# Optimization experiments

Hardware: AMD Instinct MI355X
Metric: run time of the kernel (lower is better)

The kernel has to match this reference:

```python
import jax, jax.numpy as jnp
import numpy as np
import math

NUM_HEADS = 16
HEAD_DIM = 128
ROPE_BASE = 10000.0


def setup_inputs() -> dict:
    key = jax.random.key(0)
    ks = jax.random.split(key, 6)
    B, S, H = 2, 2048, 2048
    hidden_states = jax.random.normal(ks[0], (B, S, H), dtype=jnp.float32) * 0.02
    # causal additive mask, shape (B, 1, S, S)
    neg = jnp.finfo(jnp.float32).min
    causal = jnp.where(jnp.tril(jnp.ones((S, S), dtype=bool)), 0.0, neg).astype(jnp.float32)
    attention_mask = jnp.broadcast_to(causal[None, None], (B, 1, S, S))
    position_ids = jnp.broadcast_to(jnp.arange(S, dtype=jnp.int64)[None], (B, S))
    scale = 1.0 / math.sqrt(H)
    Wq = jax.random.normal(ks[1], (H, H), dtype=jnp.float32) * scale
    Wk = jax.random.normal(ks[2], (H, H), dtype=jnp.float32) * scale
    Wv = jax.random.normal(ks[3], (H, H), dtype=jnp.float32) * scale
    Wo = jax.random.normal(ks[4], (H, H), dtype=jnp.float32) * scale
    return {"hidden_states": hidden_states, "attention_mask": attention_mask,
            "position_ids": position_ids, "Wq": Wq, "Wk": Wk, "Wv": Wv, "Wo": Wo}


def _rotate_half(x):
    x1, x2 = jnp.split(x, 2, axis=-1)
    return jnp.concatenate((-x2, x1), axis=-1)


def reference(hidden_states, attention_mask, position_ids, Wq, Wk, Wv, Wo):
    B, S, H = hidden_states.shape
    nh, hd = NUM_HEADS, HEAD_DIM

    def shape_heads(x):  # (B,S,H) -> (B,nh,S,hd)
        return x.reshape(B, S, nh, hd).transpose(0, 2, 1, 3)

    q = shape_heads(hidden_states @ Wq.T)
    k = shape_heads(hidden_states @ Wk.T)
    v = shape_heads(hidden_states @ Wv.T)

    kv_seq_len = S  # no past_key_value
    # rotary table: (kv_seq_len, hd)
    inv_freq = 1.0 / (ROPE_BASE ** (jnp.arange(0, hd, 2, dtype=jnp.float32) / hd))
    t = jnp.arange(kv_seq_len, dtype=jnp.float32)
    freqs = jnp.einsum('i,j->ij', t, inv_freq)
    emb = jnp.concatenate((freqs, freqs), axis=-1)
    # gather-based RoPE == table lookup at position_ids: (B,S,hd) -> (B,1,S,hd)
    cos = jnp.cos(emb)[position_ids][:, None]
    sin = jnp.sin(emb)[position_ids][:, None]

    q = q * cos + _rotate_half(q) * sin
    k = k * cos + _rotate_half(k) * sin

    scores = jnp.einsum('bhqd,bhkd->bhqk', q, k) / math.sqrt(hd)
    scores = scores + attention_mask
    scores = jnp.maximum(scores, jnp.finfo(scores.dtype).min)
    probs = jax.nn.softmax(scores.astype(jnp.float32), axis=-1).astype(q.dtype)
    attn = jnp.einsum('bhqk,bhkd->bhqd', probs, v)  # (B,nh,S,hd)
    attn = attn.transpose(0, 2, 1, 3).reshape(B, S, H)
    return attn @ Wo.T
```

## Files before the change

kernel.cpp:

```cpp
#include <hip/hip_runtime.h>
#include <hip/hip_bf16.h>
#include <cstdint>

#define SQ    2048
#define HDIM  2048
#define NH    16
#define HD    128
#define BATCH 2
#define MTOK  (BATCH*SQ)

typedef unsigned short u16;
typedef unsigned int   u32;
typedef __bf16 bf16x8 __attribute__((ext_vector_type(8)));
typedef float  f32x4  __attribute__((ext_vector_type(4)));
typedef float  f32x16 __attribute__((ext_vector_type(16)));
typedef unsigned short u16x4 __attribute__((ext_vector_type(4)));
typedef unsigned int   u32x4 __attribute__((ext_vector_type(4)));

__device__ __forceinline__ u16 f2b(float f) {
  union { float f; unsigned u; } v; v.f = f;
  return (u16)((v.u + 0x7fffu + ((v.u >> 16) & 1u)) >> 16);
}
__device__ __forceinline__ float b2f(u16 b) {
  union { unsigned u; float f; } v; v.u = ((unsigned)b) << 16;
  return v.f;
}

#define GLD_LDS16(gp, lp) __builtin_amdgcn_global_load_lds( \
    (const __attribute__((address_space(1))) uint32_t*)(gp), \
    (__attribute__((address_space(3))) uint32_t*)(lp), 16, 0, 0)

__device__ __forceinline__ f32x16 zero16() {
  f32x16 v;
#pragma unroll
  for (int i = 0; i < 16; ++i) v[i] = 0.f;
  return v;
}

__global__ __launch_bounds__(256) void conv_bf16(const float* __restrict__ in,
                                                 u16* __restrict__ out, int n4) {
  int i = blockIdx.x * 256 + threadIdx.x;
  if (i >= n4) return;
  float4 v = ((const float4*)in)[i];
  u16x4 o;
  o.x = f2b(v.x); o.y = f2b(v.y); o.z = f2b(v.z); o.w = f2b(v.w);
  *(u16x4*)(out + (size_t)i * 4) = o;
}

__global__ __launch_bounds__(256) void conv_w4(const float* __restrict__ w0,
                                               const float* __restrict__ w1,
                                               const float* __restrict__ w2,
                                               const float* __restrict__ w3,
                                               u16* o0, u16* o1, u16* o2, u16* o3) {
  int i = blockIdx.x * 256 + threadIdx.x;
  int sel = blockIdx.y;
  const float* in = sel == 0 ? w0 : sel == 1 ? w1 : sel == 2 ? w2 : w3;
  u16* out = sel == 0 ? o0 : sel == 1 ? o1 : sel == 2 ? o2 : o3;
  float4 v = ((const float4*)in)[i];
  u16x4 o;
  o.x = f2b(v.x); o.y = f2b(v.y); o.z = f2b(v.z); o.w = f2b(v.w);
  *(u16x4*)(out + (size_t)i * 4) = o;
}

__global__ __launch_bounds__(256) void addk(const float* __restrict__ a,
                                            const float* __restrict__ b,
                                            float* __restrict__ o) {
  int i = blockIdx.x * 256 + threadIdx.x;
  float4 x = ((const float4*)a)[i], y = ((const float4*)b)[i];
  float4 r; r.x = x.x + y.x; r.y = x.y + y.y; r.z = x.z + y.z; r.w = x.w + y.w;
  ((float4*)o)[i] = r;
}

__global__ void rope_table_k(float* __restrict__ ct, float* __restrict__ st) {
  int s = blockIdx.x, j = threadIdx.x;
  float invf = expf(-(float)j * (9.210340371976184f / 64.0f));
  float ang = (float)s * invf;
  ct[s * 64 + j] = cosf(ang);
  st[s * 64 + j] = sinf(ang);
}

__global__ __launch_bounds__(256) void rope_apply2(u16* __restrict__ Xq,
                                                   u16* __restrict__ Xk,
                                                   const float* __restrict__ ct,
                                                   const float* __restrict__ st) {
  u16* X = blockIdx.y ? Xk : Xq;
  int idx = blockIdx.x * 256 + threadIdx.x;
  int j = idx & 63;
  int row = idx >> 6;
  int s = row & (SQ - 1);
  size_t base = (size_t)row * HD;
  float x1 = b2f(X[base + j]), x2 = b2f(X[base + j + 64]);
  float c = ct[s * 64 + j], sn = st[s * 64 + j];
  X[base + j]      = f2b(x1 * c - x2 * sn);
  X[base + j + 64] = f2b(x2 * c + x1 * sn);
}

template<int OUT>
__global__ __launch_bounds__(512, 1)
void gemm8m(const u16* __restrict__ A, const u16* __restrict__ W0,
            const u16* __restrict__ W1, const u16* __restrict__ W2,
            u16* __restrict__ oQ, u16* __restrict__ oK, u16* __restrict__ oV,
            float* __restrict__ oF, float* __restrict__ oF2, int nt) {
  __shared__ u16 Ah[2][2][128 * 64];
  __shared__ u16 Bh[2][2][128 * 64];
  const int tid = threadIdx.x, lane = tid & 63, w = tid >> 6;
  const int wm = w >> 2, wn = w & 3;
  const int gx = gridDim.x;
  const int lin = blockIdx.y * gx + blockIdx.x;
  const int cpx = (gx * gridDim.y) >> 3;
  const int swz = (lin & 7) * cpx + (lin >> 3);
  const int bx = swz % gx, by = swz / gx;
  const int m0 = by * 256;
  const int n0g = bx * 256;
  const int kbase = (OUT == 1) ? (int)blockIdx.z * 1024 : 0;
  int sel; const u16* Bw; int nloc;
  if (OUT == 0) {
    sel = n0g >> 11;
    Bw = (sel == 0) ? W0 : (sel == 1) ? W1 : W2;
    nloc = n0g & 2047;
  } else {
    sel = 0; Bw = W0; nloc = n0g;
  }
  float* dstF = (OUT == 1) ? (blockIdx.z ? oF2 : oF) : oF;

  u32 aoff[2][2], boff[2][2];
#pragma unroll
  for (int h = 0; h < 2; ++h) {
#pragma unroll
    for (int l = 0; l < 2; ++l) {
      int c = l * 512 + tid, ra = c >> 3, sl = c & 7;
      int r = ((ra >> 6) << 7) + h * 64 + (ra & 63);
      aoff[h][l] = (u32)((m0 + r) * HDIM + kbase + ((sl ^ (ra & 7)) * 8));
      int col = nloc + ((ra >> 5) * 64) + h * 32 + (ra & 31);
      boff[h][l] = (u32)(col * HDIM + kbase + ((sl ^ (ra & 7)) * 8));
    }
  }
  auto stageA = [&](int buf, int h, int k0) {
#pragma unroll
    for (int l = 0; l < 2; ++l)
      GLD_LDS16(A + (size_t)aoff[h][l] + k0, &Ah[buf][h][(l * 512 + tid) * 8]);
  };
  auto stageB = [&](int buf, int h, int k0) {
#pragma unroll
    for (int l = 0; l < 2; ++l)
      GLD_LDS16(Bw + (size_t)boff[h][l] + k0, &Bh[buf][h][(l * 512 + tid) * 8]);
  };

  f32x4 acc[8][4];
#pragma unroll
  for (int i = 0; i < 8; ++i)
#pragma unroll
    for (int j = 0; j < 4; ++j) acc[i][j] = (f32x4){0.f, 0.f, 0.f, 0.f};

  const int l15 = lane & 15, hi4 = lane >> 4;
  const int swr = (l15 & 7) << 4;

  bf16x8 afv0[4][2], afv1[4][2];
  bf16x8 bfv0[2][2], bfv1[2][2];

  auto readA = [&](bf16x8 (&dst)[4][2], const char* Ab) {
#pragma unroll
    for (int j = 0; j < 4; ++j)
#pragma unroll
      for (int kk = 0; kk < 2; ++kk)
        dst[j][kk] = *(const bf16x8*)(Ab + (wm * 64 + j * 16 + l15) * 128 +
                                      ((kk * 64 + hi4 * 16) ^ swr));
  };
  auto readB = [&](bf16x8 (&dst)[2][2], const char* Bb) {
#pragma unroll
    for (int j2 = 0; j2 < 2; ++j2)
#pragma unroll
      for (int kk = 0; kk < 2; ++kk)
        dst[j2][kk] = *(const bf16x8*)(Bb + (wn * 32 + j2 * 16 + l15) * 128 +
                                       ((kk * 64 + hi4 * 16) ^ swr));
  };
  auto mfq = [&](bf16x8 (&af)[4][2], bf16x8 (&bf)[2][2], int mh, int nh) {
#pragma unroll
    for (int kk = 0; kk < 2; ++kk)
#pragma unroll
      for (int j = 0; j < 4; ++j)
#pragma unroll
        for (int j2 = 0; j2 < 2; ++j2)
          acc[mh * 4 + j][nh * 2 + j2] = __builtin_amdgcn_mfma_f32_16x16x32_bf16(
              af[j][kk], bf[j2][kk], acc[mh * 4 + j][nh * 2 + j2], 0, 0, 0);
  };

  stageA(0, 0, 0); stageB(0, 0, 0); stageA(0, 1, 0); stageB(0, 1, 0);
  asm volatile("s_waitcnt vmcnt(4)" ::: "memory");
  __builtin_amdgcn_s_barrier();

  for (int t = 0; t < nt; ++t) {
    const int cur = t & 1, nb = cur ^ 1;
    const bool st = (t + 1 < nt);
    const int kn = (t + 1) * 64;
    const char* Ab0 = (const char*)&Ah[cur][0][0];
    const char* Ab1 = (const char*)&Ah[cur][1][0];
    const char* Bb0 = (const char*)&Bh[cur][0][0];
    const char* Bb1 = (const char*)&Bh[cur][1][0];

    readA(afv0, Ab0); readB(bfv0, Bb0);
    if (st) {
      stageA(nb, 0, kn); stageB(nb, 0, kn);
      asm volatile("s_waitcnt vmcnt(6)" ::: "memory");
    } else {
      asm volatile("s_waitcnt vmcnt(2)" ::: "memory");
    }
    __builtin_amdgcn_s_barrier();
    asm volatile("s_waitcnt lgkmcnt(0)" ::: "memory");
    __builtin_amdgcn_sched_barrier(0);
    __builtin_amdgcn_s_setprio(1); mfq(afv0, bfv0, 0, 0); __builtin_amdgcn_s_setprio(0);

    readA(afv1, Ab1);
    if (st) {
      stageA(nb, 1, kn);
      asm volatile("s_waitcnt vmcnt(6)" ::: "memory");
    } else {
      asm volatile("s_waitcnt vmcnt(0)" ::: "memory");
    }
    __builtin_amdgcn_s_barrier();
    asm volatile("s_waitcnt lgkmcnt(0)" ::: "memory");
    __builtin_amdgcn_sched_barrier(0);
    __builtin_amdgcn_s_setprio(1); mfq(afv1, bfv0, 1, 0); __builtin_amdgcn_s_setprio(0);

    readB(bfv1, Bb1);
    if (st) stageB(nb, 1, kn);
    __builtin_amdgcn_s_barrier();
    asm volatile("s_waitcnt lgkmcnt(0)" ::: "memory");
    __builtin_amdgcn_sched_barrier(0);
    __builtin_amdgcn_s_setprio(1); mfq(afv0, bfv1, 0, 1); __builtin_amdgcn_s_setprio(0);

    if (st) asm volatile("s_waitcnt vmcnt(4)" ::: "memory");
    __builtin_amdgcn_s_barrier();
    __builtin_amdgcn_s_setprio(1); mfq(afv1, bfv1, 1, 1); __builtin_amdgcn_s_setprio(0);
  }

  const int cl = l15, rg = hi4 * 4;
#pragma unroll
  for (int mi = 0; mi < 8; ++mi) {
#pragma unroll
    for (int ni = 0; ni < 4; ++ni) {
      const int mb = m0 + wm * 128 + mi * 16 + rg;
      const int n = nloc + wn * 64 + ni * 16 + cl;
      if (OUT == 1) {
#pragma unroll
        for (int r = 0; r < 4; ++r)
          dstF[(size_t)(mb + r) * HDIM + n] = acc[mi][ni][r];
      } else {
        const int h = n >> 7, d = n & 127;
        if (sel == 2) {
          const int b = mb >> 11, s = mb & (SQ - 1);
          u16x4 pk;
          pk.x = f2b(acc[mi][ni][0]); pk.y = f2b(acc[mi][ni][1]);
          pk.z = f2b(acc[mi][ni][2]); pk.w = f2b(acc[mi][ni][3]);
          *(u16x4*)&oV[((size_t)(b * NH + h) * HD + d) * SQ + s] = pk;
        } else {
          u16* O = sel ? oK : oQ;
#pragma unroll
          for (int r = 0; r < 4; ++r) {
            const int m = mb + r, b = m >> 11, s = m & (SQ - 1);
            O[((size_t)(b * NH + h) * SQ + s) * HD + d] = f2b(acc[mi][ni][r]);
          }
        }
      }
    }
  }
}

__device__ __forceinline__ void stage_kv(u16* ksb, u16* vsb,
                                         const u16* __restrict__ Kg,
                                         const u16* __restrict__ Vg,
                                         int kv0, int w, int lane) {
#pragma unroll
  for (int i = 0; i < 4; ++i) {
    int chunk = (w * 4 + i) * 64 + lane;
    int row = chunk >> 4, c16 = chunk & 15;
    int csrc = c16 ^ (row & 7);
    GLD_LDS16(Kg + (size_t)(kv0 + row) * HD + csrc * 8, ksb + (w * 4 + i) * 512);
  }
#pragma unroll
  for (int i = 0; i < 4; ++i) {
    int chunk = (w * 4 + i) * 64 + lane;
    int d = chunk >> 3, c8 = chunk & 7;
    int csrc = c8 ^ (d & 7);
    GLD_LDS16(Vg + (size_t)d * SQ + kv0 + csrc * 8, vsb + (w * 4 + i) * 512);
  }
}

#define MKPA(dst, P, off) { \
  u32 u0_, u1_, u2_, u3_; \
  asm("v_cvt_pk_bf16_f32 %0, %1, %2" : "=v"(u0_) : "v"(P[off + 0]), "v"(P[off + 1])); \
  asm("v_cvt_pk_bf16_f32 %0, %1, %2" : "=v"(u1_) : "v"(P[off + 2]), "v"(P[off + 3])); \
  asm("v_cvt_pk_bf16_f32 %0, %1, %2" : "=v"(u2_) : "v"(P[off + 4]), "v"(P[off + 5])); \
  asm("v_cvt_pk_bf16_f32 %0, %1, %2" : "=v"(u3_) : "v"(P[off + 6]), "v"(P[off + 7])); \
  u32 x0_ = (u32)__shfl_xor((int)u0_, 32, 64); \
  u32 x1_ = (u32)__shfl_xor((int)u1_, 32, 64); \
  u32 x2_ = (u32)__shfl_xor((int)u2_, 32, 64); \
  u32 x3_ = (u32)__shfl_xor((int)u3_, 32, 64); \
  u32x4 w_; \
  w_.x = hi ? x2_ : u0_; \
  w_.y = hi ? x3_ : u1_; \
  w_.z = hi ? u2_ : x0_; \
  w_.w = hi ? u3_ : x1_; \
  dst = __builtin_bit_cast(bf16x8, w_); \
}

#define PVD(oD, dblk) { \
  const int dr_ = (dblk) * 32 + l31; \
  const int sw_ = (dr_ & 7) << 4; \
  bf16x8 v0_ = *(const bf16x8*)(Vb + ((dr_ * 128 +  0 + hi * 16) ^ sw_)); \
  oD = __builtin_amdgcn_mfma_f32_32x32x16_bf16(pa[0], v0_, oD, 0, 0, 0); \
  bf16x8 v1_ = *(const bf16x8*)(Vb + ((dr_ * 128 + 32 + hi * 16) ^ sw_)); \
  oD = __builtin_amdgcn_mfma_f32_32x32x16_bf16(pa[1], v1_, oD, 0, 0, 0); \
  bf16x8 v2_ = *(const bf16x8*)(Vb + ((dr_ * 128 + 64 + hi * 16) ^ sw_)); \
  oD = __builtin_amdgcn_mfma_f32_32x32x16_bf16(pa[2], v2_, oD, 0, 0, 0); \
  bf16x8 v3_ = *(const bf16x8*)(Vb + ((dr_ * 128 + 96 + hi * 16) ^ sw_)); \
  oD = __builtin_amdgcn_mfma_f32_32x32x16_bf16(pa[3], v3_, oD, 0, 0, 0); \
}

__global__ __launch_bounds__(256, 2)
void flash_fwd2(const u16* __restrict__ Q, const u16* __restrict__ K,
                const u16* __restrict__ Vt, u16* __restrict__ Out) {
  __shared__ u16 Ks[2][64 * 128];
  __shared__ u16 Vs[2][128 * 64];
  const int tid = threadIdx.x, lane = tid & 63, w = tid >> 6;
  const int hi = lane >> 5, l31 = lane & 31;
  const int qt = 15 - (int)(blockIdx.x >> 5);
  const int bh = blockIdx.x & 31;
  const int q0 = qt * 128;
  const u16* Qg = Q + (size_t)bh * SQ * HD;
  const u16* Kg = K + (size_t)bh * SQ * HD;
  const u16* Vg = Vt + (size_t)bh * HD * SQ;
  const int qw = q0 + w * 32;
  const int qg = qw + l31;

  bf16x8 qf[8];
#pragma unroll
  for (int st = 0; st < 8; ++st)
    qf[st] = *(const bf16x8*)&Qg[(size_t)qg * HD + st * 16 + hi * 8];

  f32x16 o0 = zero16(), o1 = zero16(), o2 = zero16(), o3 = zero16();
  float lsum = 0.f;
  const float sL2E = 0.1275174446f;
  const int ktl = 2 * qt + 1;
  int cur = 0;

  stage_kv(Ks[0], Vs[0], Kg, Vg, 0, w, lane);

  for (int kt = 0; kt <= ktl; ++kt) {
    if (kt < ktl) {
      stage_kv(Ks[cur ^ 1], Vs[cur ^ 1], Kg, Vg, (kt + 1) * 64, w, lane);
      asm volatile("s_waitcnt vmcnt(8)" ::: "memory");
    } else {
      asm volatile("s_waitcnt vmcnt(0)" ::: "memory");
    }
    __builtin_amdgcn_s_barrier();

    const int kv0 = kt * 64;
    if (kv0 <= qw + 31) {
      const char* Kb = (const char*)Ks[cur];
      const char* Vb = (const char*)Vs[cur];
      f32x16 c0 = zero16(), c1 = zero16();
      const int kr0 = l31, kr1 = 32 + l31;
      const int sw0 = (kr0 & 7) << 4;
#pragma unroll
      for (int st = 0; st < 8; ++st) {
        bf16x8 k0 = *(const bf16x8*)(Kb + ((kr0 * 256 + st * 32 + hi * 16) ^ sw0));
        c0 = __builtin_amdgcn_mfma_f32_32x32x16_bf16(k0, qf[st], c0, 0, 0, 0);
        bf16x8 k1 = *(const bf16x8*)(Kb + ((kr1 * 256 + st * 32 + hi * 16) ^ sw0));
        c1 = __builtin_amdgcn_mfma_f32_32x32x16_bf16(k1, qf[st], c1, 0, 0, 0);
      }
      const bool needmask = (kv0 + 63 > qw);
      const int lim0 = qg - kv0, lim1 = lim0 - 32;
      if (needmask) {
#pragma unroll
        for (int r = 0; r < 16; ++r) {
          const int cr = (r & 3) + 8 * (r >> 2) + 4 * hi;
          float p0 = exp2f(c0[r] * sL2E);
          c0[r] = (cr <= lim0) ? p0 : 0.f;
          float p1 = exp2f(c1[r] * sL2E);
          c1[r] = (cr <= lim1) ? p1 : 0.f;
          lsum += c0[r] + c1[r];
        }
      } else {
#pragma unroll
        for (int r = 0; r < 16; ++r) {
          c0[r] = exp2f(c0[r] * sL2E);
          c1[r] = exp2f(c1[r] * sL2E);
          lsum += c0[r] + c1[r];
        }
      }
      bf16x8 pa[4];
      MKPA(pa[0], c0, 0); MKPA(pa[1], c0, 8);
      MKPA(pa[2], c1, 0); MKPA(pa[3], c1, 8);
      PVD(o0, 0) PVD(o1, 1) PVD(o2, 2) PVD(o3, 3)
    }
    __builtin_amdgcn_s_barrier();
    cur ^= 1;
  }

  float ltot = lsum + __shfl_xor(lsum, 32, 64);
  float invl = 1.f / ltot;
  const int b = bh >> 4, h = bh & 15;
#pragma unroll
  for (int g = 0; g < 4; ++g) {
#pragma unroll
    for (int j = 0; j < 4; ++j) {
      const int r = g * 4 + j;
      const int cr = g * 8 + 4 * hi + j;
      float inv = __shfl(invl, cr, 64);
      const int s = q0 + w * 32 + cr;
      size_t rb = ((size_t)(b * SQ + s)) * HDIM + h * HD;
      Out[rb +  0 + l31] = f2b(o0[r] * inv);
      Out[rb + 32 + l31] = f2b(o1[r] * inv);
      Out[rb + 64 + l31] = f2b(o2[r] * inv);
      Out[rb + 96 + l31] = f2b(o3[r] * inv);
    }
  }
}

extern "C" void kernel_launch(void* const* d_in, const int* in_sizes, int n_in,
                              void* d_out, int out_size, void* d_ws, size_t ws_size,
                              hipStream_t stream) {
  const float* hs = (const float*)d_in[0];
  const float* Wq = (const float*)d_in[3];
  const float* Wk = (const float*)d_in[4];
  const float* Wv = (const float*)d_in[5];
  const float* Wo = (const float*)d_in[6];

  char* ws = (char*)d_ws;
  u16* XB  = (u16*)(ws);
  u16* WQB = (u16*)(ws + (size_t)(16 << 20));
  u16* WKB = (u16*)(ws + (size_t)(24 << 20));
  u16* WVB = (u16*)(ws + (size_t)(32 << 20));
  u16* WOB = (u16*)(ws + (size_t)(40 << 20));
  u16* QR  = (u16*)(ws + (size_t)(48 << 20));
  u16* KR  = (u16*)(ws + (size_t)(64 << 20));
  u16* VT  = (u16*)(ws + (size_t)(80 << 20));
  u16* ATT = (u16*)(ws + (size_t)(96 << 20));
  float* CT = (float*)(ws + (size_t)(112 << 20));
  float* ST = (float*)(ws + (size_t)(112 << 20) + (1 << 19));
  float* P0 = (float*)(ws);
  float* P1 = (float*)(ws + (size_t)(48 << 20));

  conv_bf16<<<8192, 256, 0, stream>>>(hs, XB, 2097152);
  conv_w4<<<dim3(4096, 4), 256, 0, stream>>>(Wq, Wk, Wv, Wo, WQB, WKB, WVB, WOB);
  rope_table_k<<<SQ, 64, 0, stream>>>(CT, ST);

  gemm8m<0><<<dim3(24, 16), 512, 0, stream>>>(XB, WQB, WKB, WVB,
                                              QR, KR, VT, nullptr, nullptr, 32);

  rope_apply2<<<dim3(16384, 2), 256, 0, stream>>>(QR, KR, CT, ST);

  flash_fwd2<<<512, 256, 0, stream>>>(QR, KR, VT, ATT);

  gemm8m<1><<<dim3(8, 16, 2), 512, 0, stream>>>(ATT, WOB, nullptr, nullptr,
                                                nullptr, nullptr, nullptr,
                                                P0, P1, 16);
  addk<<<8192, 256, 0, stream>>>(P0, P1, (float*)d_out);
}
```

Measured before the change: 276.3 us.

## Split K/V staging in flash kernel, single-buffer V loaded after PV

Separates K and V tile loads in the attention kernel. K stays double-buffered while V becomes single-buffered and is fetched for the next tile after the PV step, with an extra barrier and waitcnt between QK and PV. This cuts LDS use per block, possibly allowing higher occupancy, and overlaps the V load with the next QK compute. The K swizzle also widens from 8 to 16 rows to reduce bank conflicts. In exchange it adds a barrier per iteration and can expose V load latency.

Measured after the change: 281.0 us. About the same (+1.7%).

```diff
diff --git a/kernel.cpp b/kernel.cpp
--- a/kernel.cpp
+++ b/kernel.cpp
@@ -266,17 +266,18 @@
   }
 }
 
-__device__ __forceinline__ void stage_kv(u16* ksb, u16* vsb,
-                                         const u16* __restrict__ Kg,
-                                         const u16* __restrict__ Vg,
+__device__ __forceinline__ void stage_k4(u16* ksb, const u16* __restrict__ Kg,
                                          int kv0, int w, int lane) {
 #pragma unroll
   for (int i = 0; i < 4; ++i) {
     int chunk = (w * 4 + i) * 64 + lane;
     int row = chunk >> 4, c16 = chunk & 15;
-    int csrc = c16 ^ (row & 7);
+    int csrc = c16 ^ (row & 15);
     GLD_LDS16(Kg + (size_t)(kv0 + row) * HD + csrc * 8, ksb + (w * 4 + i) * 512);
   }
+}
+__device__ __forceinline__ void stage_v4(u16* vsb, const u16* __restrict__ Vg,
+                                         int kv0, int w, int lane) {
 #pragma unroll
   for (int i = 0; i < 4; ++i) {
     int chunk = (w * 4 + i) * 64 + lane;
@@ -318,10 +319,10 @@
 }
 
 __global__ __launch_bounds__(256, 2)
-void flash_fwd2(const u16* __restrict__ Q, const u16* __restrict__ K,
+void flash_fwd4(const u16* __restrict__ Q, const u16* __restrict__ K,
                 const u16* __restrict__ Vt, u16* __restrict__ Out) {
   __shared__ u16 Ks[2][64 * 128];
-  __shared__ u16 Vs[2][128 * 64];
+  __shared__ u16 Vs[128 * 64];
   const int tid = threadIdx.x, lane = tid & 63, w = tid >> 6;
   const int hi = lane >> 5, l31 = lane & 31;
   const int qt = 15 - (int)(blockIdx.x >> 5);
@@ -344,24 +345,26 @@
   const int ktl = 2 * qt + 1;
   int cur = 0;
 
-  stage_kv(Ks[0], Vs[0], Kg, Vg, 0, w, lane);
+  stage_k4(Ks[0], Kg, 0, w, lane);
+  stage_v4(Vs, Vg, 0, w, lane);
 
   for (int kt = 0; kt <= ktl; ++kt) {
     if (kt < ktl) {
-      stage_kv(Ks[cur ^ 1], Vs[cur ^ 1], Kg, Vg, (kt + 1) * 64, w, lane);
+      stage_k4(Ks[cur ^ 1], Kg, (kt + 1) * 64, w, lane);
       asm volatile("s_waitcnt vmcnt(8)" ::: "memory");
     } else {
-      asm volatile("s_waitcnt vmcnt(0)" ::: "memory");
+      asm volatile("s_waitcnt vmcnt(4)" ::: "memory");
     }
     __builtin_amdgcn_s_barrier();
 
     const int kv0 = kt * 64;
-    if (kv0 <= qw + 31) {
+    const bool act = (kv0 <= qw + 31);
+    bf16x8 pa[4];
+    if (act) {
       const char* Kb = (const char*)Ks[cur];
-      const char* Vb = (const char*)Vs[cur];
       f32x16 c0 = zero16(), c1 = zero16();
       const int kr0 = l31, kr1 = 32 + l31;
-      const int sw0 = (kr0 & 7) << 4;
+      const int sw0 = (l31 & 15) << 4;
 #pragma unroll
       for (int st = 0; st < 8; ++st) {
         bf16x8 k0 = *(const bf16x8*)(Kb + ((kr0 * 256 + st * 32 + hi * 16) ^ sw0));
@@ -389,12 +392,18 @@
           lsum += c0[r] + c1[r];
         }
       }
-      bf16x8 pa[4];
       MKPA(pa[0], c0, 0); MKPA(pa[1], c0, 8);
       MKPA(pa[2], c1, 0); MKPA(pa[3], c1, 8);
+    }
+    if (kt < ktl) asm volatile("s_waitcnt vmcnt(4)" ::: "memory");
+    else          asm volatile("s_waitcnt vmcnt(0)" ::: "memory");
+    __builtin_amdgcn_s_barrier();
+    if (act) {
+      const char* Vb = (const char*)Vs;
       PVD(o0, 0) PVD(o1, 1) PVD(o2, 2) PVD(o3, 3)
     }
     __builtin_amdgcn_s_barrier();
+    if (kt < ktl) stage_v4(Vs, Vg, (kt + 1) * 64, w, lane);
     cur ^= 1;
   }
 
@@ -451,7 +460,7 @@
 
   rope_apply2<<<dim3(16384, 2), 256, 0, stream>>>(QR, KR, CT, ST);
 
-  flash_fwd2<<<512, 256, 0, stream>>>(QR, KR, VT, ATT);
+  flash_fwd4<<<512, 256, 0, stream>>>(QR, KR, VT, ATT);
 
   gemm8m<1><<<dim3(8, 16, 2), 512, 0, stream>>>(ATT, WOB, nullptr, nullptr,
                                                 nullptr, nullptr, nullptr,
```

## Fuse RoPE into QKV GEMM epilogue via LDS exchange; widen K swizzle

Applied to the files above, without the earlier changes.

Removes the separate rope_apply2 pass over Q and K. The QKV GEMM epilogue now stages each accumulator half-tile into LDS, reads the partner element at d^64, applies the rotation with the cos/sin tables and writes bf16 Q/K directly. This saves a full read-modify-write of Q and K in global memory and one kernel launch, at the cost of extra barriers and LDS traffic in the epilogue. It also widens the K tile's LDS XOR swizzle from 8 to 16 row phases in the flash kernel to reduce bank conflicts.

Result: faster. 270.1 us (median of 3 runs) (-2.3%).

```diff
diff --git a/kernel.cpp b/kernel.cpp
--- a/kernel.cpp
+++ b/kernel.cpp
@@ -79,30 +79,17 @@
   st[s * 64 + j] = sinf(ang);
 }
 
-__global__ __launch_bounds__(256) void rope_apply2(u16* __restrict__ Xq,
-                                                   u16* __restrict__ Xk,
-                                                   const float* __restrict__ ct,
-                                                   const float* __restrict__ st) {
-  u16* X = blockIdx.y ? Xk : Xq;
-  int idx = blockIdx.x * 256 + threadIdx.x;
-  int j = idx & 63;
-  int row = idx >> 6;
-  int s = row & (SQ - 1);
-  size_t base = (size_t)row * HD;
-  float x1 = b2f(X[base + j]), x2 = b2f(X[base + j + 64]);
-  float c = ct[s * 64 + j], sn = st[s * 64 + j];
-  X[base + j]      = f2b(x1 * c - x2 * sn);
-  X[base + j + 64] = f2b(x2 * c + x1 * sn);
-}
-
 template<int OUT>
 __global__ __launch_bounds__(512, 1)
 void gemm8m(const u16* __restrict__ A, const u16* __restrict__ W0,
             const u16* __restrict__ W1, const u16* __restrict__ W2,
             u16* __restrict__ oQ, u16* __restrict__ oK, u16* __restrict__ oV,
-            float* __restrict__ oF, float* __restrict__ oF2, int nt) {
-  __shared__ u16 Ah[2][2][128 * 64];
-  __shared__ u16 Bh[2][2][128 * 64];
+            float* __restrict__ oF, float* __restrict__ oF2,
+            const float* __restrict__ ct, const float* __restrict__ st,
+            int nt) {
+  __shared__ char smem[131072];
+  u16 (*Ah)[2][128 * 64] = (u16(*)[2][128 * 64])smem;
+  u16 (*Bh)[2][128 * 64] = (u16(*)[2][128 * 64])(smem + 65536);
   const int tid = threadIdx.x, lane = tid & 63, w = tid >> 6;
   const int wm = w >> 2, wn = w & 3;
   const int gx = gridDim.x;
@@ -191,7 +178,7 @@
 
   for (int t = 0; t < nt; ++t) {
     const int cur = t & 1, nb = cur ^ 1;
-    const bool st = (t + 1 < nt);
+    const bool st2 = (t + 1 < nt);
     const int kn = (t + 1) * 64;
     const char* Ab0 = (const char*)&Ah[cur][0][0];
     const char* Ab1 = (const char*)&Ah[cur][1][0];
@@ -199,7 +186,7 @@
     const char* Bb1 = (const char*)&Bh[cur][1][0];
 
     readA(afv0, Ab0); readB(bfv0, Bb0);
-    if (st) {
+    if (st2) {
       stageA(nb, 0, kn); stageB(nb, 0, kn);
       asm volatile("s_waitcnt vmcnt(6)" ::: "memory");
     } else {
@@ -211,7 +198,7 @@
     __builtin_amdgcn_s_setprio(1); mfq(afv0, bfv0, 0, 0); __builtin_amdgcn_s_setprio(0);
 
     readA(afv1, Ab1);
-    if (st) {
+    if (st2) {
       stageA(nb, 1, kn);
       asm volatile("s_waitcnt vmcnt(6)" ::: "memory");
     } else {
@@ -223,18 +210,61 @@
     __builtin_amdgcn_s_setprio(1); mfq(afv1, bfv0, 1, 0); __builtin_amdgcn_s_setprio(0);
 
     readB(bfv1, Bb1);
-    if (st) stageB(nb, 1, kn);
+    if (st2) stageB(nb, 1, kn);
     __builtin_amdgcn_s_barrier();
     asm volatile("s_waitcnt lgkmcnt(0)" ::: "memory");
     __builtin_amdgcn_sched_barrier(0);
     __builtin_amdgcn_s_setprio(1); mfq(afv0, bfv1, 0, 1); __builtin_amdgcn_s_setprio(0);
 
-    if (st) asm volatile("s_waitcnt vmcnt(4)" ::: "memory");
+    if (st2) asm volatile("s_waitcnt vmcnt(4)" ::: "memory");
     __builtin_amdgcn_s_barrier();
     __builtin_amdgcn_s_setprio(1); mfq(afv1, bfv1, 1, 1); __builtin_amdgcn_s_setprio(0);
   }
 
   const int cl = l15, rg = hi4 * 4;
+  if (OUT == 0 && sel != 2) {
+    float* Ls = (float*)smem;
+    u16* O = sel ? oK : oQ;
+#pragma unroll
+    for (int mh = 0; mh < 2; ++mh) {
+      __builtin_amdgcn_s_barrier();
+      if (wm == mh) {
+#pragma unroll
+        for (int mi = 0; mi < 8; ++mi)
+#pragma unroll
+          for (int ni = 0; ni < 4; ++ni) {
+            const int n = wn * 64 + ni * 16 + cl;
+#pragma unroll
+            for (int r = 0; r < 4; ++r) {
+              const int lrow = mi * 16 + rg + r;
+              Ls[lrow * 256 + (n ^ (((lrow >> 2) & 3) << 4))] = acc[mi][ni][r];
+            }
+          }
+      }
+      __builtin_amdgcn_s_barrier();
+      if (wm == mh) {
+#pragma unroll
+        for (int mi = 0; mi < 8; ++mi)
+#pragma unroll
+          for (int ni = 0; ni < 4; ++ni) {
+            const int n = wn * 64 + ni * 16 + cl;
+            const int ng = nloc + n, h = ng >> 7, d = ng & 127, j = d & 63;
+#pragma unroll
+            for (int r = 0; r < 4; ++r) {
+              const int lrow = mi * 16 + rg + r;
+              const int m = m0 + mh * 128 + lrow;
+              const int b = m >> 11, s = m & (SQ - 1);
+              float x  = acc[mi][ni][r];
+              float xo = Ls[lrow * 256 + ((n ^ 64) ^ (((lrow >> 2) & 3) << 4))];
+              float c = ct[s * 64 + j], sn = st[s * 64 + j];
+              float res = (d < 64) ? (x * c - xo * sn) : (x * c + xo * sn);
+              O[((size_t)(b * NH + h) * SQ + s) * HD + d] = f2b(res);
+            }
+          }
+      }
+    }
+    return;
+  }
 #pragma unroll
   for (int mi = 0; mi < 8; ++mi) {
 #pragma unroll
@@ -247,20 +277,11 @@
           dstF[(size_t)(mb + r) * HDIM + n] = acc[mi][ni][r];
       } else {
         const int h = n >> 7, d = n & 127;
-        if (sel == 2) {
-          const int b = mb >> 11, s = mb & (SQ - 1);
-          u16x4 pk;
-          pk.x = f2b(acc[mi][ni][0]); pk.y = f2b(acc[mi][ni][1]);
-          pk.z = f2b(acc[mi][ni][2]); pk.w = f2b(acc[mi][ni][3]);
-          *(u16x4*)&oV[((size_t)(b * NH + h) * HD + d) * SQ + s] = pk;
-        } else {
-          u16* O = sel ? oK : oQ;
-#pragma unroll
-          for (int r = 0; r < 4; ++r) {
-            const int m = mb + r, b = m >> 11, s = m & (SQ - 1);
-            O[((size_t)(b * NH + h) * SQ + s) * HD + d] = f2b(acc[mi][ni][r]);
-          }
-        }
+        const int b = mb >> 11, s = mb & (SQ - 1);
+        u16x4 pk;
+        pk.x = f2b(acc[mi][ni][0]); pk.y = f2b(acc[mi][ni][1]);
+        pk.z = f2b(acc[mi][ni][2]); pk.w = f2b(acc[mi][ni][3]);
+        *(u16x4*)&oV[((size_t)(b * NH + h) * HD + d) * SQ + s] = pk;
       }
     }
   }
@@ -274,7 +295,7 @@
   for (int i = 0; i < 4; ++i) {
     int chunk = (w * 4 + i) * 64 + lane;
     int row = chunk >> 4, c16 = chunk & 15;
-    int csrc = c16 ^ (row & 7);
+    int csrc = c16 ^ (row & 15);
     GLD_LDS16(Kg + (size_t)(kv0 + row) * HD + csrc * 8, ksb + (w * 4 + i) * 512);
   }
 #pragma unroll
@@ -361,7 +382,7 @@
       const char* Vb = (const char*)Vs[cur];
       f32x16 c0 = zero16(), c1 = zero16();
       const int kr0 = l31, kr1 = 32 + l31;
-      const int sw0 = (kr0 & 7) << 4;
+      const int sw0 = (l31 & 15) << 4;
 #pragma unroll
       for (int st = 0; st < 8; ++st) {
         bf16x8 k0 = *(const bf16x8*)(Kb + ((kr0 * 256 + st * 32 + hi * 16) ^ sw0));
@@ -447,14 +468,13 @@
   rope_table_k<<<SQ, 64, 0, stream>>>(CT, ST);
 
   gemm8m<0><<<dim3(24, 16), 512, 0, stream>>>(XB, WQB, WKB, WVB,
-                                              QR, KR, VT, nullptr, nullptr, 32);
-
-  rope_apply2<<<dim3(16384, 2), 256, 0, stream>>>(QR, KR, CT, ST);
+                                              QR, KR, VT, nullptr, nullptr,
+                                              CT, ST, 32);
 
   flash_fwd2<<<512, 256, 0, stream>>>(QR, KR, VT, ATT);
 
   gemm8m<1><<<dim3(8, 16, 2), 512, 0, stream>>>(ATT, WOB, nullptr, nullptr,
                                                 nullptr, nullptr, nullptr,
-                                                P0, P1, 16);
+                                                P0, P1, nullptr, nullptr, 16);
   addk<<<8192, 256, 0, stream>>>(P0, P1, (float*)d_out);
 }
```
